# Kernel tuning notes

Measured on AMD Instinct MI355X. Metric: run time of the kernel, lower is better.

The kernel has to match this reference:

```python
import jax, jax.numpy as jnp
import numpy as np
import math

# ---- module config (from init_kwargs) ----
IRREPS = [(0, 8), (1, 8), (2, 8), (3, 8), (4, 8)]  # (l, multiplicity)
MAX_M = max(l for l, _ in IRREPS)
TOTAL_DIM = sum(m * (2 * l + 1) for l, m in IRREPS)  # 200
BATCH, CHANNELS = 2048, 128

# ---- constant per-l change-of-axis matrices A_l = D_real^l(Rx(-pi/2)) ----
# Wigner ZYZ decomposition in the real spherical-harmonic basis:
#   D^l(a,b,g) = Z(a) @ A_l @ Z(b) @ A_l^T @ Z(g)
# where Z(theta) is the sparse real Z-rotation (cos/sin m*theta blocks).

def _small_d(l, beta):
    d = np.zeros((2 * l + 1, 2 * l + 1))
    for mp in range(-l, l + 1):
        for m in range(-l, l + 1):
            pref = math.sqrt(math.factorial(l + mp) * math.factorial(l - mp)
                             * math.factorial(l + m) * math.factorial(l - m))
            tot = 0.0
            for s in range(max(0, m - mp), min(l + m, l - mp) + 1):
                den = (math.factorial(l + m - s) * math.factorial(s)
                       * math.factorial(mp - m + s) * math.factorial(l - mp - s))
                tot += ((-1.0) ** (mp - m + s) / den
                        * math.cos(beta / 2) ** (2 * l + m - mp - 2 * s)
                        * math.sin(beta / 2) ** (mp - m + 2 * s))
            d[mp + l, m + l] = pref * tot
    return d

def _U(l):
    # complex->real spherical harmonic change of basis
    U = np.zeros((2 * l + 1, 2 * l + 1), dtype=np.complex128)
    U[l, l] = 1.0
    for m in range(1, l + 1):
        U[l + m, l + m] = (-1.0) ** m / math.sqrt(2)
        U[l + m, l - m] = 1.0 / math.sqrt(2)
        U[l - m, l - m] = 1j / math.sqrt(2)
        U[l - m, l + m] = -1j * (-1.0) ** m / math.sqrt(2)
    return U

def _A(l):
    # real Wigner-D of Rx(-pi/2) = Rz(-pi/2) Ry(-pi/2) Rz(pi/2)
    a, b, g = -np.pi / 2, -np.pi / 2, np.pi / 2
    mv = np.arange(-l, l + 1)
    Dc = np.exp(-1j * mv[:, None] * a) * _small_d(l, b) * np.exp(-1j * mv[None, :] * g)
    U = _U(l)
    return np.real(U @ Dc @ U.conj().T)

A_MATS = {l: jnp.asarray(_A(l), dtype=jnp.float32) for l in sorted({l for l, _ in IRREPS})}


def _sincos(key, batch):
    theta = jax.random.uniform(key, (batch,), minval=0.0, maxval=2 * np.pi)
    m = jnp.arange(MAX_M + 1, dtype=jnp.float32)          # (max_m+1,)
    mt = theta[:, None] * m[None, :]                       # (B, max_m+1)
    return jnp.stack([jnp.sin(mt), jnp.cos(mt)], axis=-1).astype(jnp.float32)


def setup_inputs() -> dict:
    key = jax.random.key(0)
    k0, k1, k2, k3 = jax.random.split(key, 4)
    return {
        "input": jax.random.normal(k0, (BATCH, TOTAL_DIM, CHANNELS), dtype=jnp.float32),
        "sincos_alpha": _sincos(k1, BATCH),
        "sincos_beta": _sincos(k2, BATCH),
        "sincos_gamma": _sincos(k3, BATCH),
    }


def _zrot(x, sincos, l):
    # x: (B, mult, 2l+1, C); sincos: (B, max_m+1, 2) with [...,0]=sin(m t), [...,1]=cos(m t)
    # out[m] = cos(m t) x[m] + sin(m t) x[-m]   (m = -l..l; sin odd, cos even)
    m = jnp.arange(-l, l + 1)
    am = jnp.abs(m)
    cos = sincos[:, am, 1]                                  # (B, 2l+1)
    sin = jnp.sign(m).astype(x.dtype) * sincos[:, am, 0]    # (B, 2l+1)
    return cos[:, None, :, None] * x + sin[:, None, :, None] * x[:, :, ::-1, :]


def reference(input, sincos_alpha, sincos_beta, sincos_gamma):
    B, _, C = input.shape
    outs = []
    off = 0
    for l, mult in IRREPS:
        d = 2 * l + 1
        seg = input[:, off:off + mult * d, :].reshape(B, mult, d, C)
        off += mult * d
        A = A_MATS[l]
        y = _zrot(seg, sincos_gamma, l)
        y = jnp.einsum('ij,bmjc->bmic', A.T, y)
        y = _zrot(y, sincos_beta, l)
        y = jnp.einsum('ij,bmjc->bmic', A, y)
        y = _zrot(y, sincos_alpha, l)
        outs.append(y.reshape(B, mult * d, C))
    return jnp.concatenate(outs, axis=1)
```

## Files before the change

kernel.cpp:

```cpp
#include <hip/hip_runtime.h>


#define NBATCH 2048

__device__ __forceinline__ int urow_entries(int L, int p, int* c, double* r, int* ph) {
  const double s2 = 0.70710678118654752440;
  int m = p - L;
  if (m == 0) { c[0] = L; r[0] = 1.0; ph[0] = 0; return 1; }
  if (m > 0) {
    c[0] = L + m; r[0] = ((m & 1) ? -s2 : s2); ph[0] = 0;
    c[1] = L - m; r[1] = s2;                  ph[1] = 0;
    return 2;
  }
  int mu = -m;
  c[0] = L - mu; r[0] = s2;                    ph[0] = 1;
  c[1] = L + mu; r[1] = ((mu & 1) ? s2 : -s2); ph[1] = 1;
  return 2;
}

template <int L>
__device__ __forceinline__ void build_R_impl(const float* __restrict__ sa,
                                             const float* __restrict__ sb,
                                             const float* __restrict__ sg,
                                             float* __restrict__ R_all,
                                             double* dsm, float* As,
                                             int blockX, int tid) {
  constexpr int D = 2 * L + 1;

  if (tid < D * D) {
    int jp = tid / D, jm = tid % D;
    int mp = jp - L, m = jm - L;
    double f[9];
    f[0] = 1.0;
    for (int i = 1; i < 9; ++i) f[i] = f[i - 1] * (double)i;
    double pref = sqrt(f[L + mp] * f[L - mp] * f[L + m] * f[L - m]);
    const double c  =  0.70710678118654752440;
    const double sn = -0.70710678118654752440;
    double tot = 0.0;
    int s0 = (m - mp) > 0 ? (m - mp) : 0;
    int s1 = (L + m) < (L - mp) ? (L + m) : (L - mp);
    for (int s = s0; s <= s1; ++s) {
      double den  = f[L + m - s] * f[s] * f[mp - m + s] * f[L - mp - s];
      double term = (((mp - m + s) & 1) ? -1.0 : 1.0) / den;
      int e1 = 2 * L + m - mp - 2 * s;
      int e2 = mp - m + 2 * s;
      double p1 = 1.0, p2 = 1.0;
      for (int t = 0; t < e1; ++t) p1 *= c;
      for (int t = 0; t < e2; ++t) p2 *= sn;
      tot += term * p1 * p2;
    }
    dsm[tid] = pref * tot;
  }
  __syncthreads();

  if (tid < D * D) {
    int p = tid / D, q = tid % D;
    int c1[2], ph1[2], c2[2], ph2[2];
    double r1[2], r2[2];
    int n1 = urow_entries(L, p, c1, r1, ph1);
    int n2 = urow_entries(L, q, c2, r2, ph2);
    double acc = 0.0;
    for (int a = 0; a < n1; ++a)
      for (int bq = 0; bq < n2; ++bq) {
        int tp = ((c1[a] - c2[bq]) + ph1[a] - ph2[bq] + 12) & 3;
        double v = r1[a] * r2[bq] * dsm[c1[a] * D + c2[bq]];
        if (tp == 0) acc += v;
        else if (tp == 2) acc -= v;
      }
    As[tid] = (float)acc;
  }
  __syncthreads();

  int b = blockX * 256 + tid;
  float ca[D], sav[D], cb[D], sbv[D];
#pragma unroll
  for (int i = 0; i < D; ++i) {
    int mm = i - L;
    int am = mm < 0 ? -mm : mm;
    float sgn = (float)((mm > 0) - (mm < 0));
    ca[i] = sa[b * 10 + am * 2 + 1];
    sav[i] = sgn * sa[b * 10 + am * 2 + 0];
    cb[i] = sb[b * 10 + am * 2 + 1];
    sbv[i] = sgn * sb[b * 10 + am * 2 + 0];
  }
  constexpr int offR[5] = {0, 1, 10, 35, 84};
  float* Rout = R_all + (size_t)b * 165 + offR[L];
#pragma unroll
  for (int k = 0; k < D; ++k) {
    int mmk = k - L;
    int amk = mmk < 0 ? -mmk : mmk;
    float sgnk = (float)((mmk > 0) - (mmk < 0));
    float cgk = sg[b * 10 + amk * 2 + 1];
    float sgk = sgnk * sg[b * 10 + amk * 2 + 0];
    float c2v[D], c3v[D], c4v[D];
#pragma unroll
    for (int i = 0; i < D; ++i)
      c2v[i] = cgk * As[k * D + i] - sgk * As[(2 * L - k) * D + i];
#pragma unroll
    for (int i = 0; i < D; ++i) c3v[i] = cb[i] * c2v[i] + sbv[i] * c2v[2 * L - i];
#pragma unroll
    for (int p = 0; p < D; ++p) {
      float s = 0.f;
#pragma unroll
      for (int i = 0; i < D; ++i) s = fmaf(As[p * D + i], c3v[i], s);
      c4v[p] = s;
    }
#pragma unroll
    for (int p = 0; p < D; ++p)
      Rout[p * D + k] = ca[p] * c4v[p] + sav[p] * c4v[2 * L - p];
  }
}

__global__ __launch_bounds__(256) void build_R_kernel(const float* __restrict__ sa,
                                                      const float* __restrict__ sb,
                                                      const float* __restrict__ sg,
                                                      float* __restrict__ R_all) {
  __shared__ double dsm[81];
  __shared__ float As[81];
  int tid = threadIdx.x;
  switch (blockIdx.y) {
    case 0: build_R_impl<0>(sa, sb, sg, R_all, dsm, As, blockIdx.x, tid); break;
    case 1: build_R_impl<1>(sa, sb, sg, R_all, dsm, As, blockIdx.x, tid); break;
    case 2: build_R_impl<2>(sa, sb, sg, R_all, dsm, As, blockIdx.x, tid); break;
    case 3: build_R_impl<3>(sa, sb, sg, R_all, dsm, As, blockIdx.x, tid); break;
    case 4: build_R_impl<4>(sa, sb, sg, R_all, dsm, As, blockIdx.x, tid); break;
  }
}

template <int L>
__device__ __forceinline__ void apply_seg(const float4* __restrict__ ip0,
                                          float4* __restrict__ op0,
                                          const float* __restrict__ Rl, int mBase) {
  constexpr int D = 2 * L + 1;
#pragma unroll
  for (int mi = 0; mi < 4; ++mi) {
    int m = mBase + mi;
    const float4* ip = ip0 + m * D * 32;
    float4* op = op0 + m * D * 32;
    float4 x[D];
#pragma unroll
    for (int j = 0; j < D; ++j) x[j] = ip[j * 32];
#pragma unroll
    for (int i = 0; i < D; ++i) {
      float r = Rl[i * D];
      float4 a;
      a.x = r * x[0].x; a.y = r * x[0].y; a.z = r * x[0].z; a.w = r * x[0].w;
#pragma unroll
      for (int j = 1; j < D; ++j) {
        r = Rl[i * D + j];
        a.x = fmaf(r, x[j].x, a.x);
        a.y = fmaf(r, x[j].y, a.y);
        a.z = fmaf(r, x[j].z, a.z);
        a.w = fmaf(r, x[j].w, a.w);
      }
      op[i * 32] = a;
    }
  }
}

__global__ __launch_bounds__(256) void apply_R_kernel(const float* __restrict__ in,
                                                      const float* __restrict__ R_all,
                                                      float* __restrict__ out) {
  __shared__ float Rs[8][165];
  int tid = threadIdx.x;
  int g = tid >> 5;
  int q = tid & 31;
  int b = blockIdx.x * 8 + g;
  for (int t = q; t < 165; t += 32) Rs[g][t] = R_all[(size_t)b * 165 + t];
  __syncthreads();
  int mBase = blockIdx.y * 4;
  const float4* ib = (const float4*)in + (size_t)b * 6400 + q;
  float4* ob = (float4*)out + (size_t)b * 6400 + q;
  const float* Rg = Rs[g];
  apply_seg<0>(ib + 0 * 32,   ob + 0 * 32,   Rg + 0,  mBase);
  apply_seg<1>(ib + 8 * 32,   ob + 8 * 32,   Rg + 1,  mBase);
  apply_seg<2>(ib + 32 * 32,  ob + 32 * 32,  Rg + 10, mBase);
  apply_seg<3>(ib + 72 * 32,  ob + 72 * 32,  Rg + 35, mBase);
  apply_seg<4>(ib + 128 * 32, ob + 128 * 32, Rg + 84, mBase);
}

extern "C" void kernel_launch(void* const* d_in, const int* in_sizes, int n_in,
                              void* d_out, int out_size, void* d_ws, size_t ws_size,
                              hipStream_t stream) {
  const float* in = (const float*)d_in[0];
  const float* sa = (const float*)d_in[1];
  const float* sb = (const float*)d_in[2];
  const float* sg = (const float*)d_in[3];
  float* out = (float*)d_out;
  float* R_all = (float*)d_ws;

  build_R_kernel<<<dim3(8, 5), 256, 0, stream>>>(sa, sb, sg, R_all);
  apply_R_kernel<<<dim3(NBATCH / 8, 2), 256, 0, stream>>>(in, R_all, out);
}
```

Before: 373.3 us.

## Fuse rotation-matrix build into apply kernel, one block per batch element

Merges the two kernels into one. Each block now handles one batch element: it computes the constant A matrices, builds the per-sample Wigner matrix in shared memory with threads working in parallel over matrix entries, and then applies it, with each warp taking one multiplicity slot. This removes the workspace round trip for R and one kernel launch. In exchange, every block redundantly recomputes the double-precision small-d and A matrices and goes through several barriers before any streaming work begins, which could delay the memory-bound phase.

```diff
diff --git a/kernel.cpp b/kernel.cpp
--- a/kernel.cpp
+++ b/kernel.cpp
@@ -2,6 +2,30 @@
 
 
 #define NBATCH 2048
+
+__device__ __forceinline__ double small_d_elem(int L, int jp, int jm) {
+  int mp = jp - L, m = jm - L;
+  double f[10];
+  f[0] = 1.0;
+  for (int i = 1; i < 10; ++i) f[i] = f[i - 1] * (double)i;
+  double pref = sqrt(f[L + mp] * f[L - mp] * f[L + m] * f[L - m]);
+  const double c  =  0.70710678118654752440;
+  const double sn = -0.70710678118654752440;
+  double tot = 0.0;
+  int s0 = (m - mp) > 0 ? (m - mp) : 0;
+  int s1 = (L + m) < (L - mp) ? (L + m) : (L - mp);
+  for (int s = s0; s <= s1; ++s) {
+    double den  = f[L + m - s] * f[s] * f[mp - m + s] * f[L - mp - s];
+    double term = (((mp - m + s) & 1) ? -1.0 : 1.0) / den;
+    int e1 = 2 * L + m - mp - 2 * s;
+    int e2 = mp - m + 2 * s;
+    double p1 = 1.0, p2 = 1.0;
+    for (int t = 0; t < e1; ++t) p1 *= c;
+    for (int t = 0; t < e2; ++t) p2 *= sn;
+    tot += term * p1 * p2;
+  }
+  return pref * tot;
+}
 
 __device__ __forceinline__ int urow_entries(int L, int p, int* c, double* r, int* ph) {
   const double s2 = 0.70710678118654752440;
@@ -9,7 +33,7 @@
   if (m == 0) { c[0] = L; r[0] = 1.0; ph[0] = 0; return 1; }
   if (m > 0) {
     c[0] = L + m; r[0] = ((m & 1) ? -s2 : s2); ph[0] = 0;
-    c[1] = L - m; r[1] = s2;                  ph[1] = 0;
+    c[1] = L - m; r[1] = s2;                   ph[1] = 0;
     return 2;
   }
   int mu = -m;
@@ -18,165 +42,118 @@
   return 2;
 }
 
-template <int L>
-__device__ __forceinline__ void build_R_impl(const float* __restrict__ sa,
-                                             const float* __restrict__ sb,
-                                             const float* __restrict__ sg,
-                                             float* __restrict__ R_all,
-                                             double* dsm, float* As,
-                                             int blockX, int tid) {
+template <int L, int RB, int RO>
+__device__ __forceinline__ void apply_block(const float4* __restrict__ ib,
+                                            float4* __restrict__ ob,
+                                            const float* __restrict__ Rsm, int g) {
   constexpr int D = 2 * L + 1;
+  const float4* ip = ib + (RB + g * D) * 32;
+  float4* op = ob + (RB + g * D) * 32;
+  const float* R = Rsm + RO;
+  float4 x[D];
+#pragma unroll
+  for (int j = 0; j < D; ++j) x[j] = ip[j * 32];
+#pragma unroll
+  for (int i = 0; i < D; ++i) {
+    float r = R[i * D];
+    float4 a;
+    a.x = r * x[0].x; a.y = r * x[0].y; a.z = r * x[0].z; a.w = r * x[0].w;
+#pragma unroll
+    for (int j = 1; j < D; ++j) {
+      r = R[i * D + j];
+      a.x = fmaf(r, x[j].x, a.x);
+      a.y = fmaf(r, x[j].y, a.y);
+      a.z = fmaf(r, x[j].z, a.z);
+      a.w = fmaf(r, x[j].w, a.w);
+    }
+    op[i * 32] = a;
+  }
+}
 
-  if (tid < D * D) {
-    int jp = tid / D, jm = tid % D;
-    int mp = jp - L, m = jm - L;
-    double f[9];
-    f[0] = 1.0;
-    for (int i = 1; i < 9; ++i) f[i] = f[i - 1] * (double)i;
-    double pref = sqrt(f[L + mp] * f[L - mp] * f[L + m] * f[L - m]);
-    const double c  =  0.70710678118654752440;
-    const double sn = -0.70710678118654752440;
-    double tot = 0.0;
-    int s0 = (m - mp) > 0 ? (m - mp) : 0;
-    int s1 = (L + m) < (L - mp) ? (L + m) : (L - mp);
-    for (int s = s0; s <= s1; ++s) {
-      double den  = f[L + m - s] * f[s] * f[mp - m + s] * f[L - mp - s];
-      double term = (((mp - m + s) & 1) ? -1.0 : 1.0) / den;
-      int e1 = 2 * L + m - mp - 2 * s;
-      int e2 = mp - m + 2 * s;
-      double p1 = 1.0, p2 = 1.0;
-      for (int t = 0; t < e1; ++t) p1 *= c;
-      for (int t = 0; t < e2; ++t) p2 *= sn;
-      tot += term * p1 * p2;
-    }
-    dsm[tid] = pref * tot;
-  }
+__global__ __launch_bounds__(256, 4) void wigner_fused_kernel(
+    const float* __restrict__ in, const float* __restrict__ sa,
+    const float* __restrict__ sb, const float* __restrict__ sg,
+    float* __restrict__ out) {
+  __shared__ double dsm[165];
+  __shared__ float Asm[165];
+  __shared__ float Msm[165];
+  __shared__ float Rsm[165];
+
+  const int t = threadIdx.x;
+  const int b = blockIdx.x;
+
+  int L = 0, off = 0;
+  if (t >= 84) { L = 4; off = 84; }
+  else if (t >= 35) { L = 3; off = 35; }
+  else if (t >= 10) { L = 2; off = 10; }
+  else if (t >= 1)  { L = 1; off = 1; }
+  const int D = 2 * L + 1;
+  const int loc = t - off;
+  const int i = loc / D;
+  const int j = loc - i * D;
+
+  if (t < 165) dsm[t] = small_d_elem(L, i, j);
   __syncthreads();
 
-  if (tid < D * D) {
-    int p = tid / D, q = tid % D;
+  if (t < 165) {
     int c1[2], ph1[2], c2[2], ph2[2];
     double r1[2], r2[2];
-    int n1 = urow_entries(L, p, c1, r1, ph1);
-    int n2 = urow_entries(L, q, c2, r2, ph2);
+    int n1 = urow_entries(L, i, c1, r1, ph1);
+    int n2 = urow_entries(L, j, c2, r2, ph2);
     double acc = 0.0;
     for (int a = 0; a < n1; ++a)
       for (int bq = 0; bq < n2; ++bq) {
         int tp = ((c1[a] - c2[bq]) + ph1[a] - ph2[bq] + 12) & 3;
-        double v = r1[a] * r2[bq] * dsm[c1[a] * D + c2[bq]];
+        double v = r1[a] * r2[bq] * dsm[off + c1[a] * D + c2[bq]];
         if (tp == 0) acc += v;
         else if (tp == 2) acc -= v;
       }
-    As[tid] = (float)acc;
+    Asm[t] = (float)acc;
   }
   __syncthreads();
 
-  int b = blockX * 256 + tid;
-  float ca[D], sav[D], cb[D], sbv[D];
-#pragma unroll
-  for (int i = 0; i < D; ++i) {
-    int mm = i - L;
-    int am = mm < 0 ? -mm : mm;
-    float sgn = (float)((mm > 0) - (mm < 0));
-    ca[i] = sa[b * 10 + am * 2 + 1];
-    sav[i] = sgn * sa[b * 10 + am * 2 + 0];
-    cb[i] = sb[b * 10 + am * 2 + 1];
-    sbv[i] = sgn * sb[b * 10 + am * 2 + 0];
+  if (t < 165) {
+    float acc = 0.0f;
+    for (int ii = 0; ii < D; ++ii) {
+      int mm = ii - L;
+      int am = mm < 0 ? -mm : mm;
+      float sgn = (float)((mm > 0) - (mm < 0));
+      float cb = sb[b * 10 + am * 2 + 1];
+      float sv = sgn * sb[b * 10 + am * 2 + 0];
+      acc += Asm[off + i * D + ii] *
+             (cb * Asm[off + j * D + ii] + sv * Asm[off + j * D + (2 * L - ii)]);
+    }
+    Msm[t] = acc;
   }
-  constexpr int offR[5] = {0, 1, 10, 35, 84};
-  float* Rout = R_all + (size_t)b * 165 + offR[L];
-#pragma unroll
-  for (int k = 0; k < D; ++k) {
-    int mmk = k - L;
-    int amk = mmk < 0 ? -mmk : mmk;
-    float sgnk = (float)((mmk > 0) - (mmk < 0));
+  __syncthreads();
+
+  if (t < 165) {
+    int p = i, k = j;
+    int mmp = p - L, amp = mmp < 0 ? -mmp : mmp;
+    float sgp = (float)((mmp > 0) - (mmp < 0));
+    float cap = sa[b * 10 + amp * 2 + 1];
+    float sav = sgp * sa[b * 10 + amp * 2 + 0];
+    int mmk = k - L, amk = mmk < 0 ? -mmk : mmk;
+    float sgk = (float)((mmk > 0) - (mmk < 0));
     float cgk = sg[b * 10 + amk * 2 + 1];
-    float sgk = sgnk * sg[b * 10 + amk * 2 + 0];
-    float c2v[D], c3v[D], c4v[D];
-#pragma unroll
-    for (int i = 0; i < D; ++i)
-      c2v[i] = cgk * As[k * D + i] - sgk * As[(2 * L - k) * D + i];
-#pragma unroll
-    for (int i = 0; i < D; ++i) c3v[i] = cb[i] * c2v[i] + sbv[i] * c2v[2 * L - i];
-#pragma unroll
-    for (int p = 0; p < D; ++p) {
-      float s = 0.f;
-#pragma unroll
-      for (int i = 0; i < D; ++i) s = fmaf(As[p * D + i], c3v[i], s);
-      c4v[p] = s;
-    }
-#pragma unroll
-    for (int p = 0; p < D; ++p)
-      Rout[p * D + k] = ca[p] * c4v[p] + sav[p] * c4v[2 * L - p];
+    float sgv = sgk * sg[b * 10 + amk * 2 + 0];
+    float m00 = Msm[off + p * D + k];
+    float m01 = Msm[off + p * D + (2 * L - k)];
+    float m10 = Msm[off + (2 * L - p) * D + k];
+    float m11 = Msm[off + (2 * L - p) * D + (2 * L - k)];
+    Rsm[t] = cap * (cgk * m00 - sgv * m01) + sav * (cgk * m10 - sgv * m11);
   }
-}
+  __syncthreads();
 
-__global__ __launch_bounds__(256) void build_R_kernel(const float* __restrict__ sa,
-                                                      const float* __restrict__ sb,
-                                                      const float* __restrict__ sg,
-                                                      float* __restrict__ R_all) {
-  __shared__ double dsm[81];
-  __shared__ float As[81];
-  int tid = threadIdx.x;
-  switch (blockIdx.y) {
-    case 0: build_R_impl<0>(sa, sb, sg, R_all, dsm, As, blockIdx.x, tid); break;
-    case 1: build_R_impl<1>(sa, sb, sg, R_all, dsm, As, blockIdx.x, tid); break;
-    case 2: build_R_impl<2>(sa, sb, sg, R_all, dsm, As, blockIdx.x, tid); break;
-    case 3: build_R_impl<3>(sa, sb, sg, R_all, dsm, As, blockIdx.x, tid); break;
-    case 4: build_R_impl<4>(sa, sb, sg, R_all, dsm, As, blockIdx.x, tid); break;
-  }
-}
-
-template <int L>
-__device__ __forceinline__ void apply_seg(const float4* __restrict__ ip0,
-                                          float4* __restrict__ op0,
-                                          const float* __restrict__ Rl, int mBase) {
-  constexpr int D = 2 * L + 1;
-#pragma unroll
-  for (int mi = 0; mi < 4; ++mi) {
-    int m = mBase + mi;
-    const float4* ip = ip0 + m * D * 32;
-    float4* op = op0 + m * D * 32;
-    float4 x[D];
-#pragma unroll
-    for (int j = 0; j < D; ++j) x[j] = ip[j * 32];
-#pragma unroll
-    for (int i = 0; i < D; ++i) {
-      float r = Rl[i * D];
-      float4 a;
-      a.x = r * x[0].x; a.y = r * x[0].y; a.z = r * x[0].z; a.w = r * x[0].w;
-#pragma unroll
-      for (int j = 1; j < D; ++j) {
-        r = Rl[i * D + j];
-        a.x = fmaf(r, x[j].x, a.x);
-        a.y = fmaf(r, x[j].y, a.y);
-        a.z = fmaf(r, x[j].z, a.z);
-        a.w = fmaf(r, x[j].w, a.w);
-      }
-      op[i * 32] = a;
-    }
-  }
-}
-
-__global__ __launch_bounds__(256) void apply_R_kernel(const float* __restrict__ in,
-                                                      const float* __restrict__ R_all,
-                                                      float* __restrict__ out) {
-  __shared__ float Rs[8][165];
-  int tid = threadIdx.x;
-  int g = tid >> 5;
-  int q = tid & 31;
-  int b = blockIdx.x * 8 + g;
-  for (int t = q; t < 165; t += 32) Rs[g][t] = R_all[(size_t)b * 165 + t];
-  __syncthreads();
-  int mBase = blockIdx.y * 4;
+  const int g = t >> 5;
+  const int q = t & 31;
   const float4* ib = (const float4*)in + (size_t)b * 6400 + q;
   float4* ob = (float4*)out + (size_t)b * 6400 + q;
-  const float* Rg = Rs[g];
-  apply_seg<0>(ib + 0 * 32,   ob + 0 * 32,   Rg + 0,  mBase);
-  apply_seg<1>(ib + 8 * 32,   ob + 8 * 32,   Rg + 1,  mBase);
-  apply_seg<2>(ib + 32 * 32,  ob + 32 * 32,  Rg + 10, mBase);
-  apply_seg<3>(ib + 72 * 32,  ob + 72 * 32,  Rg + 35, mBase);
-  apply_seg<4>(ib + 128 * 32, ob + 128 * 32, Rg + 84, mBase);
+  apply_block<0, 0,   0 >(ib, ob, Rsm, g);
+  apply_block<1, 8,   1 >(ib, ob, Rsm, g);
+  apply_block<2, 32,  10>(ib, ob, Rsm, g);
+  apply_block<3, 72,  35>(ib, ob, Rsm, g);
+  apply_block<4, 128, 84>(ib, ob, Rsm, g);
 }
 
 extern "C" void kernel_launch(void* const* d_in, const int* in_sizes, int n_in,
@@ -187,8 +164,6 @@
   const float* sb = (const float*)d_in[2];
   const float* sg = (const float*)d_in[3];
   float* out = (float*)d_out;
-  float* R_all = (float*)d_ws;
 
-  build_R_kernel<<<dim3(8, 5), 256, 0, stream>>>(sa, sb, sg, R_all);
-  apply_R_kernel<<<dim3(NBATCH / 8, 2), 256, 0, stream>>>(in, R_all, out);
+  wigner_fused_kernel<<<dim3(NBATCH), 256, 0, stream>>>(in, sa, sb, sg, out);
 }
```

After: 358.0 us. 1.04x faster.
